# Kernel tuning notes

Hardware: AMD Instinct MI355X
Metric: run time of the kernel (lower is better)

Reference implementation:

```python
import jax, jax.numpy as jnp
import numpy as np

EPS = 0.1          # perturbation scale (init kwarg eps)
NORM_EPS = 1e-12   # torch F.normalize clamp


def spmm(row, col, val, x, n):
    # sparse COO matmul: out[row] += val * x[col]
    return jax.ops.segment_sum(val[:, None] * x[col], row, num_segments=n)


def setup_inputs() -> dict:
    key = jax.random.key(0)
    ks = jax.random.split(key, 6)
    U, I, D, NNZ, L = 100000, 50000, 64, 2000000, 3
    N = U + I
    return {
        "user_emb": jax.random.normal(ks[0], (U, D), dtype=jnp.float32),
        "item_emb": jax.random.normal(ks[1], (I, D), dtype=jnp.float32),
        "adj_row": jax.random.randint(ks[2], (NNZ,), 0, N, dtype=jnp.int64),
        "adj_col": jax.random.randint(ks[3], (NNZ,), 0, N, dtype=jnp.int64),
        "adj_val": jax.random.uniform(ks[4], (NNZ,), dtype=jnp.float32),
        "noise": jax.random.uniform(ks[5], (L, N, D), dtype=jnp.float32),
    }


def reference(user_emb, item_emb, adj_row, adj_col, adj_val, noise):
    U = user_emb.shape[0]
    N = U + item_emb.shape[0]
    L = noise.shape[0]
    ego = jnp.concatenate([user_emb, item_emb], axis=0)  # [N, D]
    layer_sum = jnp.zeros_like(ego)
    for k in range(L):
        ego = spmm(adj_row, adj_col, adj_val, ego, N)
        # perturbed branch: ego += sign(ego) * L2-normalize(noise_k) * eps
        rn = noise[k]
        rn = rn / jnp.maximum(jnp.linalg.norm(rn, axis=-1, keepdims=True), NORM_EPS)
        ego = ego + jnp.sign(ego) * rn * EPS
        layer_sum = layer_sum + ego
    all_emb = layer_sum / L  # mean over stacked layers
    return all_emb[:U], all_emb[U:]
```

## Files before the change

### kernel.cpp

```cpp
#include <hip/hip_runtime.h>
#include <hip/hip_fp16.h>

#define DDIM 64
#define EPS 0.1f
#define NORM_EPS 1e-12f

__global__ void init_zero_kernel(const float* __restrict__ user, const float* __restrict__ item,
                                 float* __restrict__ egoA, float* __restrict__ egoB,
                                 int UD, int ND) {
    int i = blockIdx.x * blockDim.x + threadIdx.x;
    if (i < ND) {
        egoA[i] = (i < UD) ? user[i] : item[i - UD];
        egoB[i] = 0.0f;
    }
}

__global__ void zero_int_kernel(int* __restrict__ p, int n) {
    int i = blockIdx.x * blockDim.x + threadIdx.x;
    if (i < n) p[i] = 0;
}

__global__ void hist_kernel(const int* __restrict__ row, int* __restrict__ cnt,
                            int* __restrict__ pos, int nnz) {
    int e = blockIdx.x * blockDim.x + threadIdx.x;
    if (e < nnz) pos[e] = atomicAdd(&cnt[row[e]], 1);
}

__global__ void scan1_kernel(const int* __restrict__ cnt, int* __restrict__ partial,
                             int* __restrict__ bsums, int n) {
    __shared__ int s[1024];
    int i = blockIdx.x * 1024 + threadIdx.x;
    int v = (i < n) ? cnt[i] : 0;
    s[threadIdx.x] = v;
    __syncthreads();
    for (int off = 1; off < 1024; off <<= 1) {
        int t = (threadIdx.x >= off) ? s[threadIdx.x - off] : 0;
        __syncthreads();
        s[threadIdx.x] += t;
        __syncthreads();
    }
    if (i < n) partial[i] = s[threadIdx.x];
    if (threadIdx.x == 1023) bsums[blockIdx.x] = s[1023];
}

__global__ void scan2_kernel(int* __restrict__ bsums, int nb) {
    if (blockIdx.x == 0 && threadIdx.x == 0) {
        int run = 0;
        for (int b = 0; b < nb; ++b) { int t = bsums[b]; bsums[b] = run; run += t; }
    }
}

__global__ void scan3_serialbs_kernel(const int* __restrict__ partial, const int* __restrict__ bsums,
                                      int* __restrict__ rowptr, int n) {
    int i = blockIdx.x * 1024 + threadIdx.x;
    if (i < n) rowptr[i + 1] = partial[i] + bsums[blockIdx.x];
    if (i == 0) rowptr[0] = 0;
}

__global__ void scan3_fused_kernel(const int* __restrict__ partial, const int* __restrict__ bsums,
                                   int* __restrict__ rowptr, int n, int nb) {
    __shared__ int s[1024];
    int t = threadIdx.x;
    s[t] = (t < nb && t < (int)blockIdx.x) ? bsums[t] : 0;
    __syncthreads();
    #pragma unroll
    for (int off = 512; off > 0; off >>= 1) {
        if (t < off) s[t] += s[t + off];
        __syncthreads();
    }
    int base = s[0];
    int i = blockIdx.x * 1024 + t;
    if (i < n) rowptr[i + 1] = partial[i] + base;
    if (i == 0) rowptr[0] = 0;
}

__global__ void scatter_kernel(const int* __restrict__ row, const int* __restrict__ col,
                               const float* __restrict__ val, const int* __restrict__ rowptr,
                               const int* __restrict__ pos, int2* __restrict__ edges, int nnz) {
    int e = blockIdx.x * blockDim.x + threadIdx.x;
    if (e < nnz) {
        int r = row[e];
        edges[rowptr[r] + pos[e]] = make_int2(col[e], __float_as_int(val[e]));
    }
}

__device__ __forceinline__ void fma_mix8(float& f0, float& f1, float& f2, float& f3,
                                         float& f4, float& f5, float& f6, float& f7,
                                         uint4 q, float v) {
    asm("v_fma_mix_f32 %0, %8, %12, %0 op_sel:[0,0,0] op_sel_hi:[1,0,0]\n\t"
        "v_fma_mix_f32 %1, %8, %12, %1 op_sel:[1,0,0] op_sel_hi:[1,0,0]\n\t"
        "v_fma_mix_f32 %2, %9, %12, %2 op_sel:[0,0,0] op_sel_hi:[1,0,0]\n\t"
        "v_fma_mix_f32 %3, %9, %12, %3 op_sel:[1,0,0] op_sel_hi:[1,0,0]\n\t"
        "v_fma_mix_f32 %4, %10, %12, %4 op_sel:[0,0,0] op_sel_hi:[1,0,0]\n\t"
        "v_fma_mix_f32 %5, %10, %12, %5 op_sel:[1,0,0] op_sel_hi:[1,0,0]\n\t"
        "v_fma_mix_f32 %6, %11, %12, %6 op_sel:[0,0,0] op_sel_hi:[1,0,0]\n\t"
        "v_fma_mix_f32 %7, %11, %12, %7 op_sel:[1,0,0] op_sel_hi:[1,0,0]"
        : "+v"(f0), "+v"(f1), "+v"(f2), "+v"(f3),
          "+v"(f4), "+v"(f5), "+v"(f6), "+v"(f7)
        : "v"(q.x), "v"(q.y), "v"(q.z), "v"(q.w), "v"(v));
}

template <int XHALF>
__global__ void fused_layer_kernel(const int* __restrict__ rowptr, const int2* __restrict__ edges,
                                   const float4* __restrict__ xu4, const float4* __restrict__ xi4,
                                   int splitRow,
                                   const uint4* __restrict__ x16,
                                   const float4* __restrict__ noise4,
                                   uint4* __restrict__ y16, float4* __restrict__ out4,
                                   int N, int first, float invL) {
    int lane = threadIdx.x & 63;
    int wid = (blockIdx.x * blockDim.x + threadIdx.x) >> 6;
    int g   = lane >> 3;
    int sub = lane & 7;
    int r = wid * 8 + g;
    bool active = r < N;

    size_t f4idx = (size_t)r * 16 + sub * 2;

    float4 nva = make_float4(0.f,0.f,0.f,0.f), nvb = make_float4(0.f,0.f,0.f,0.f);
    float4 poa = make_float4(0.f,0.f,0.f,0.f), pob = make_float4(0.f,0.f,0.f,0.f);
    int beg = 0, end = 0;
    if (active) {
        beg = rowptr[r];
        end = rowptr[r + 1];
        nva = noise4[f4idx]; nvb = noise4[f4idx + 1];
        if (!first) { poa = out4[f4idx]; pob = out4[f4idx + 1]; }
    }

    float f0=0.f,f1=0.f,f2=0.f,f3=0.f,f4=0.f,f5=0.f,f6=0.f,f7=0.f;

    int e = beg;
    if (XHALF) {
        while (e + 2 <= end) {
            int2 ed0 = edges[e];
            int2 ed1 = edges[e + 1];
            uint4 q0 = x16[(size_t)ed0.x * 8 + sub];
            uint4 q1 = x16[(size_t)ed1.x * 8 + sub];
            fma_mix8(f0,f1,f2,f3,f4,f5,f6,f7, q0, __int_as_float(ed0.y));
            fma_mix8(f0,f1,f2,f3,f4,f5,f6,f7, q1, __int_as_float(ed1.y));
            e += 2;
        }
        if (e < end) {
            int2 ed = edges[e];
            uint4 q = x16[(size_t)ed.x * 8 + sub];
            fma_mix8(f0,f1,f2,f3,f4,f5,f6,f7, q, __int_as_float(ed.y));
        }
    } else {
        while (e < end) {
            int2 ed = edges[e];
            float v = __int_as_float(ed.y);
            const float4* s = (ed.x < splitRow) ? (xu4 + (size_t)ed.x * 16)
                                                : (xi4 + (size_t)(ed.x - splitRow) * 16);
            float4 a = s[sub * 2], b = s[sub * 2 + 1];
            f0 = fmaf(v, a.x, f0); f1 = fmaf(v, a.y, f1);
            f2 = fmaf(v, a.z, f2); f3 = fmaf(v, a.w, f3);
            f4 = fmaf(v, b.x, f4); f5 = fmaf(v, b.y, f5);
            f6 = fmaf(v, b.z, f6); f7 = fmaf(v, b.w, f7);
            ++e;
        }
    }

    float sq = nva.x*nva.x + nva.y*nva.y + nva.z*nva.z + nva.w*nva.w
             + nvb.x*nvb.x + nvb.y*nvb.y + nvb.z*nvb.z + nvb.w*nvb.w;
    #pragma unroll
    for (int off = 1; off <= 4; off <<= 1) sq += __shfl_xor(sq, off, 64);
    float scale = EPS / fmaxf(sqrtf(sq), NORM_EPS);

    float acc[8] = {f0,f1,f2,f3,f4,f5,f6,f7};
    float nse[8] = {nva.x,nva.y,nva.z,nva.w,nvb.x,nvb.y,nvb.z,nvb.w};
    float po[8]  = {poa.x,poa.y,poa.z,poa.w,pob.x,pob.y,pob.z,pob.w};
    float ep[8];
    #pragma unroll
    for (int i = 0; i < 8; ++i) {
        float s = (acc[i] > 0.f) ? 1.f : ((acc[i] < 0.f) ? -1.f : 0.f);
        ep[i] = acc[i] + s * nse[i] * scale;
    }

    if (active) {
        if (y16) {
            __half2 h0 = __floats2half2_rn(ep[0], ep[1]);
            __half2 h1 = __floats2half2_rn(ep[2], ep[3]);
            __half2 h2 = __floats2half2_rn(ep[4], ep[5]);
            __half2 h3 = __floats2half2_rn(ep[6], ep[7]);
            uint4 st;
            st.x = *reinterpret_cast<unsigned*>(&h0);
            st.y = *reinterpret_cast<unsigned*>(&h1);
            st.z = *reinterpret_cast<unsigned*>(&h2);
            st.w = *reinterpret_cast<unsigned*>(&h3);
            y16[(size_t)r * 8 + sub] = st;
        }
        float4 oa, ob;
        if (first) {
            oa = make_float4(ep[0]*invL, ep[1]*invL, ep[2]*invL, ep[3]*invL);
            ob = make_float4(ep[4]*invL, ep[5]*invL, ep[6]*invL, ep[7]*invL);
        } else {
            oa = make_float4(fmaf(ep[0],invL,po[0]), fmaf(ep[1],invL,po[1]),
                             fmaf(ep[2],invL,po[2]), fmaf(ep[3],invL,po[3]));
            ob = make_float4(fmaf(ep[4],invL,po[4]), fmaf(ep[5],invL,po[5]),
                             fmaf(ep[6],invL,po[6]), fmaf(ep[7],invL,po[7]));
        }
        out4[f4idx] = oa;
        out4[f4idx + 1] = ob;
    }
}

__global__ void spmm_kernel(const int* __restrict__ row, const int* __restrict__ col,
                            const float* __restrict__ val, const float* __restrict__ x,
                            float* __restrict__ y, int nnz) {
    int gtid = blockIdx.x * blockDim.x + threadIdx.x;
    int wid = gtid >> 6;
    int lane = threadIdx.x & 63;
    int nwaves = (gridDim.x * blockDim.x) >> 6;
    for (int e = wid; e < nnz; e += nwaves) {
        int r = row[e];
        int c = col[e];
        float v = val[e];
        unsafeAtomicAdd(&y[(size_t)r * DDIM + lane], v * x[(size_t)c * DDIM + lane]);
    }
}

__global__ void perturb_kernel(float* __restrict__ ego, const float* __restrict__ noise,
                               float* __restrict__ zero_buf, float* __restrict__ out,
                               int N, int first, float invL) {
    int gtid = blockIdx.x * blockDim.x + threadIdx.x;
    int wid = gtid >> 6;
    int lane = threadIdx.x & 63;
    int nwaves = (gridDim.x * blockDim.x) >> 6;
    for (int n = wid; n < N; n += nwaves) {
        size_t idx = (size_t)n * DDIM + lane;
        float nv = noise[idx];
        float sq = nv * nv;
        #pragma unroll
        for (int off = 32; off > 0; off >>= 1) sq += __shfl_xor(sq, off, 64);
        float rn = nv / fmaxf(sqrtf(sq), NORM_EPS);
        float e = ego[idx];
        float s = (e > 0.0f) ? 1.0f : ((e < 0.0f) ? -1.0f : 0.0f);
        float ep = e + s * rn * EPS;
        ego[idx] = ep;
        if (zero_buf) zero_buf[idx] = 0.0f;
        float o = ep * invL;
        out[idx] = first ? o : (out[idx] + o);
    }
}

extern "C" void kernel_launch(void* const* d_in, const int* in_sizes, int n_in,
                              void* d_out, int out_size, void* d_ws, size_t ws_size,
                              hipStream_t stream) {
    const float* user  = (const float*)d_in[0];
    const float* item  = (const float*)d_in[1];
    const int*   row   = (const int*)d_in[2];
    const int*   col   = (const int*)d_in[3];
    const float* val   = (const float*)d_in[4];
    const float* noise = (const float*)d_in[5];
    float* out = (float*)d_out;

    int UD = in_sizes[0];
    int ID = in_sizes[1];
    int ND = UD + ID;
    int N  = ND / DDIM;
    int nnz = in_sizes[2];
    int L  = in_sizes[5] / ND;
    float invL = 1.0f / (float)L;

    size_t ND_ = (size_t)ND;
    size_t ofs_rowptr  = ND_;
    size_t ofs_cnt     = ofs_rowptr + (size_t)(N + 2);
    size_t ofs_partial = ofs_cnt + (size_t)N;
    size_t ofs_bsums   = ofs_partial + (size_t)N;
    size_t ofs_pos     = ofs_bsums + 1024;
    size_t ofs_edges   = ofs_pos + (size_t)nnz;
    size_t needed = (ofs_edges + 2ull * (size_t)nnz) * 4ull;

    if (ws_size >= needed && (N % 2) == 0 && (nnz % 2) == 0 && (UD % DDIM) == 0) {
        uint4* ego16A = (uint4*)d_ws;
        uint4* ego16B = (uint4*)((char*)d_ws + 2ull * ND_);
        int* rowptr  = (int*)d_ws + ofs_rowptr;
        int* cnt     = (int*)d_ws + ofs_cnt;
        int* partial = (int*)d_ws + ofs_partial;
        int* bsums   = (int*)d_ws + ofs_bsums;
        int* pos     = (int*)d_ws + ofs_pos;
        int2* edges  = (int2*)((int*)d_ws + ofs_edges);

        int nb = (N + 1023) / 1024;

        zero_int_kernel<<<(N + 255) / 256, 256, 0, stream>>>(cnt, N);
        hist_kernel<<<(nnz + 255) / 256, 256, 0, stream>>>(row, cnt, pos, nnz);
        scan1_kernel<<<nb, 1024, 0, stream>>>(cnt, partial, bsums, N);
        if (nb <= 1024) {
            scan3_fused_kernel<<<nb, 1024, 0, stream>>>(partial, bsums, rowptr, N, nb);
        } else {
            scan2_kernel<<<1, 64, 0, stream>>>(bsums, nb);
            scan3_serialbs_kernel<<<nb, 1024, 0, stream>>>(partial, bsums, rowptr, N);
        }
        scatter_kernel<<<(nnz + 255) / 256, 256, 0, stream>>>(row, col, val, rowptr, pos, edges, nnz);

        const float4* user4 = (const float4*)user;
        const float4* item4 = (const float4*)item;
        const float4* noise4 = (const float4*)noise;
        float4* out4 = (float4*)out;
        int Urows = UD / DDIM;

        int blocks = ((N * 8) + 255) / 256;
        uint4* e16[2] = { ego16A, ego16B };
        for (int k = 0; k < L; ++k) {
            uint4* y = (k == L - 1) ? nullptr : e16[k & 1];
            const float4* nz = noise4 + (size_t)k * (ND_ / 4);
            if (k == 0) {
                fused_layer_kernel<0><<<blocks, 256, 0, stream>>>(
                    rowptr, edges, user4, item4, Urows, nullptr,
                    nz, y, out4, N, 1, invL);
            } else {
                fused_layer_kernel<1><<<blocks, 256, 0, stream>>>(
                    rowptr, edges, nullptr, nullptr, 0, (const uint4*)e16[(k - 1) & 1],
                    nz, y, out4, N, 0, invL);
            }
        }
    } else {
        float* egoA = (float*)d_ws;
        float* egoB = egoA + ND_;
        init_zero_kernel<<<(ND + 255) / 256, 256, 0, stream>>>(user, item, egoA, egoB, UD, ND);
        float* cur = egoA;
        float* nxt = egoB;
        for (int k = 0; k < L; ++k) {
            spmm_kernel<<<2048, 256, 0, stream>>>(row, col, val, cur, nxt, nnz);
            perturb_kernel<<<1024, 256, 0, stream>>>(
                nxt, noise + (size_t)k * ND_,
                (k + 1 < L) ? cur : nullptr, out, N, (k == 0) ? 1 : 0, invL);
            float* t = cur; cur = nxt; nxt = t;
        }
    }
}
```

Before: 356.6 us.

## Drop per-edge pos array and defer layer sum to final layer

The CSR build no longer stores a per-edge position array: the histogram only counts, and the scatter claims slots with an atomic decrement on the counts. The layer kernels stop reading and writing the fp32 output each layer. Each layer's fp16 embedding is kept, and the last layer adds the two earlier ones to its own result and writes the output once, which removes several full fp32 passes over N×64. The cost is fp16 precision in the summed layers, a fast path specialised to L==3, and a non-deterministic edge order within rows.

```diff
diff --git a/kernel.cpp b/kernel.cpp
--- a/kernel.cpp
+++ b/kernel.cpp
@@ -20,10 +20,9 @@
     if (i < n) p[i] = 0;
 }
 
-__global__ void hist_kernel(const int* __restrict__ row, int* __restrict__ cnt,
-                            int* __restrict__ pos, int nnz) {
+__global__ void hist_kernel(const int* __restrict__ row, int* __restrict__ cnt, int nnz) {
     int e = blockIdx.x * blockDim.x + threadIdx.x;
-    if (e < nnz) pos[e] = atomicAdd(&cnt[row[e]], 1);
+    if (e < nnz) atomicAdd(&cnt[row[e]], 1);
 }
 
 __global__ void scan1_kernel(const int* __restrict__ cnt, int* __restrict__ partial,
@@ -76,11 +75,12 @@
 
 __global__ void scatter_kernel(const int* __restrict__ row, const int* __restrict__ col,
                                const float* __restrict__ val, const int* __restrict__ rowptr,
-                               const int* __restrict__ pos, int2* __restrict__ edges, int nnz) {
+                               int* __restrict__ cnt, int2* __restrict__ edges, int nnz) {
     int e = blockIdx.x * blockDim.x + threadIdx.x;
     if (e < nnz) {
         int r = row[e];
-        edges[rowptr[r] + pos[e]] = make_int2(col[e], __float_as_int(val[e]));
+        int old = atomicSub(&cnt[r], 1);
+        edges[rowptr[r] + old - 1] = make_int2(col[e], __float_as_int(val[e]));
     }
 }
 
@@ -100,14 +100,24 @@
         : "v"(q.x), "v"(q.y), "v"(q.z), "v"(q.w), "v"(v));
 }
 
-template <int XHALF>
+__device__ __forceinline__ void h2f8(uint4 q, float o[8]) {
+    float2 t;
+    t = __half22float2(*reinterpret_cast<const __half2*>(&q.x)); o[0] = t.x; o[1] = t.y;
+    t = __half22float2(*reinterpret_cast<const __half2*>(&q.y)); o[2] = t.x; o[3] = t.y;
+    t = __half22float2(*reinterpret_cast<const __half2*>(&q.z)); o[4] = t.x; o[5] = t.y;
+    t = __half22float2(*reinterpret_cast<const __half2*>(&q.w)); o[6] = t.x; o[7] = t.y;
+}
+
+template <int XHALF, int FINAL>
 __global__ void fused_layer_kernel(const int* __restrict__ rowptr, const int2* __restrict__ edges,
                                    const float4* __restrict__ xu4, const float4* __restrict__ xi4,
                                    int splitRow,
                                    const uint4* __restrict__ x16,
                                    const float4* __restrict__ noise4,
-                                   uint4* __restrict__ y16, float4* __restrict__ out4,
-                                   int N, int first, float invL) {
+                                   uint4* __restrict__ y16,
+                                   const uint4* __restrict__ yprev0, const uint4* __restrict__ yprev1,
+                                   float4* __restrict__ out4,
+                                   int N, float invL) {
     int lane = threadIdx.x & 63;
     int wid = (blockIdx.x * blockDim.x + threadIdx.x) >> 6;
     int g   = lane >> 3;
@@ -116,15 +126,16 @@
     bool active = r < N;
 
     size_t f4idx = (size_t)r * 16 + sub * 2;
+    size_t hidx  = (size_t)r * 8 + sub;
 
     float4 nva = make_float4(0.f,0.f,0.f,0.f), nvb = make_float4(0.f,0.f,0.f,0.f);
-    float4 poa = make_float4(0.f,0.f,0.f,0.f), pob = make_float4(0.f,0.f,0.f,0.f);
+    uint4 qp0 = make_uint4(0,0,0,0), qp1 = make_uint4(0,0,0,0);
     int beg = 0, end = 0;
     if (active) {
         beg = rowptr[r];
         end = rowptr[r + 1];
         nva = noise4[f4idx]; nvb = noise4[f4idx + 1];
-        if (!first) { poa = out4[f4idx]; pob = out4[f4idx + 1]; }
+        if (FINAL) { qp0 = yprev0[hidx]; qp1 = yprev1[hidx]; }
     }
 
     float f0=0.f,f1=0.f,f2=0.f,f3=0.f,f4=0.f,f5=0.f,f6=0.f,f7=0.f;
@@ -168,7 +179,6 @@
 
     float acc[8] = {f0,f1,f2,f3,f4,f5,f6,f7};
     float nse[8] = {nva.x,nva.y,nva.z,nva.w,nvb.x,nvb.y,nvb.z,nvb.w};
-    float po[8]  = {poa.x,poa.y,poa.z,poa.w,pob.x,pob.y,pob.z,pob.w};
     float ep[8];
     #pragma unroll
     for (int i = 0; i < 8; ++i) {
@@ -177,7 +187,22 @@
     }
 
     if (active) {
-        if (y16) {
+        if (FINAL) {
+            float p0[8], p1[8];
+            h2f8(qp0, p0);
+            h2f8(qp1, p1);
+            float4 oa, ob;
+            oa.x = (p0[0] + p1[0] + ep[0]) * invL;
+            oa.y = (p0[1] + p1[1] + ep[1]) * invL;
+            oa.z = (p0[2] + p1[2] + ep[2]) * invL;
+            oa.w = (p0[3] + p1[3] + ep[3]) * invL;
+            ob.x = (p0[4] + p1[4] + ep[4]) * invL;
+            ob.y = (p0[5] + p1[5] + ep[5]) * invL;
+            ob.z = (p0[6] + p1[6] + ep[6]) * invL;
+            ob.w = (p0[7] + p1[7] + ep[7]) * invL;
+            out4[f4idx] = oa;
+            out4[f4idx + 1] = ob;
+        } else {
             __half2 h0 = __floats2half2_rn(ep[0], ep[1]);
             __half2 h1 = __floats2half2_rn(ep[2], ep[3]);
             __half2 h2 = __floats2half2_rn(ep[4], ep[5]);
@@ -187,20 +212,8 @@
             st.y = *reinterpret_cast<unsigned*>(&h1);
             st.z = *reinterpret_cast<unsigned*>(&h2);
             st.w = *reinterpret_cast<unsigned*>(&h3);
-            y16[(size_t)r * 8 + sub] = st;
-        }
-        float4 oa, ob;
-        if (first) {
-            oa = make_float4(ep[0]*invL, ep[1]*invL, ep[2]*invL, ep[3]*invL);
-            ob = make_float4(ep[4]*invL, ep[5]*invL, ep[6]*invL, ep[7]*invL);
-        } else {
-            oa = make_float4(fmaf(ep[0],invL,po[0]), fmaf(ep[1],invL,po[1]),
-                             fmaf(ep[2],invL,po[2]), fmaf(ep[3],invL,po[3]));
-            ob = make_float4(fmaf(ep[4],invL,po[4]), fmaf(ep[5],invL,po[5]),
-                             fmaf(ep[6],invL,po[6]), fmaf(ep[7],invL,po[7]));
-        }
-        out4[f4idx] = oa;
-        out4[f4idx + 1] = ob;
+            y16[hidx] = st;
+        }
     }
 }
 
@@ -263,28 +276,30 @@
     float invL = 1.0f / (float)L;
 
     size_t ND_ = (size_t)ND;
-    size_t ofs_rowptr  = ND_;
+    size_t ofs_rowptr  = (3 * ND_) / 2;
     size_t ofs_cnt     = ofs_rowptr + (size_t)(N + 2);
     size_t ofs_partial = ofs_cnt + (size_t)N;
     size_t ofs_bsums   = ofs_partial + (size_t)N;
-    size_t ofs_pos     = ofs_bsums + 1024;
-    size_t ofs_edges   = ofs_pos + (size_t)nnz;
+    size_t ofs_edges   = ofs_bsums + 1024;
     size_t needed = (ofs_edges + 2ull * (size_t)nnz) * 4ull;
 
-    if (ws_size >= needed && (N % 2) == 0 && (nnz % 2) == 0 && (UD % DDIM) == 0) {
-        uint4* ego16A = (uint4*)d_ws;
-        uint4* ego16B = (uint4*)((char*)d_ws + 2ull * ND_);
+    if (ws_size >= needed && (N % 2) == 0 && (UD % DDIM) == 0 && L == 3) {
+        uint4* ybase = (uint4*)d_ws;
+        size_t ystride = (size_t)N * 8;
+        uint4* y0 = ybase;
+        uint4* y1 = ybase + ystride;
+        uint4* y2 = ybase + 2 * ystride;
+        (void)y2;
         int* rowptr  = (int*)d_ws + ofs_rowptr;
         int* cnt     = (int*)d_ws + ofs_cnt;
         int* partial = (int*)d_ws + ofs_partial;
         int* bsums   = (int*)d_ws + ofs_bsums;
-        int* pos     = (int*)d_ws + ofs_pos;
         int2* edges  = (int2*)((int*)d_ws + ofs_edges);
 
         int nb = (N + 1023) / 1024;
 
         zero_int_kernel<<<(N + 255) / 256, 256, 0, stream>>>(cnt, N);
-        hist_kernel<<<(nnz + 255) / 256, 256, 0, stream>>>(row, cnt, pos, nnz);
+        hist_kernel<<<(nnz + 255) / 256, 256, 0, stream>>>(row, cnt, nnz);
         scan1_kernel<<<nb, 1024, 0, stream>>>(cnt, partial, bsums, N);
         if (nb <= 1024) {
             scan3_fused_kernel<<<nb, 1024, 0, stream>>>(partial, bsums, rowptr, N, nb);
@@ -292,29 +307,26 @@
             scan2_kernel<<<1, 64, 0, stream>>>(bsums, nb);
             scan3_serialbs_kernel<<<nb, 1024, 0, stream>>>(partial, bsums, rowptr, N);
         }
-        scatter_kernel<<<(nnz + 255) / 256, 256, 0, stream>>>(row, col, val, rowptr, pos, edges, nnz);
+        scatter_kernel<<<(nnz + 255) / 256, 256, 0, stream>>>(row, col, val, rowptr, cnt, edges, nnz);
 
         const float4* user4 = (const float4*)user;
         const float4* item4 = (const float4*)item;
         const float4* noise4 = (const float4*)noise;
         float4* out4 = (float4*)out;
         int Urows = UD / DDIM;
+        size_t nzstride = ND_ / 4;
 
         int blocks = ((N * 8) + 255) / 256;
-        uint4* e16[2] = { ego16A, ego16B };
-        for (int k = 0; k < L; ++k) {
-            uint4* y = (k == L - 1) ? nullptr : e16[k & 1];
-            const float4* nz = noise4 + (size_t)k * (ND_ / 4);
-            if (k == 0) {
-                fused_layer_kernel<0><<<blocks, 256, 0, stream>>>(
-                    rowptr, edges, user4, item4, Urows, nullptr,
-                    nz, y, out4, N, 1, invL);
-            } else {
-                fused_layer_kernel<1><<<blocks, 256, 0, stream>>>(
-                    rowptr, edges, nullptr, nullptr, 0, (const uint4*)e16[(k - 1) & 1],
-                    nz, y, out4, N, 0, invL);
-            }
-        }
+
+        fused_layer_kernel<0, 0><<<blocks, 256, 0, stream>>>(
+            rowptr, edges, user4, item4, Urows, nullptr,
+            noise4, y0, nullptr, nullptr, nullptr, N, invL);
+        fused_layer_kernel<1, 0><<<blocks, 256, 0, stream>>>(
+            rowptr, edges, nullptr, nullptr, 0, y0,
+            noise4 + nzstride, y1, nullptr, nullptr, nullptr, N, invL);
+        fused_layer_kernel<1, 1><<<blocks, 256, 0, stream>>>(
+            rowptr, edges, nullptr, nullptr, 0, y1,
+            noise4 + 2 * nzstride, nullptr, y0, y1, out4, N, invL);
     } else {
         float* egoA = (float*)d_ws;
         float* egoB = egoA + ND_;
```

New measurement: 381.5 us. 7.0% more time.
